# Kernel tuning notes

Measured on AMD Instinct MI355X. Metric: run time of the kernel, lower is better.

The kernel has to match this reference:

```python
import jax, jax.numpy as jnp
import numpy as np

N_NODES = 65536
N_EDGES = 1048576
HID = 128
NUM_FEAT = 128
NUM_LAYERS = 3
NUM_EXPERTS = 4
NUM_GRAPHS = 512
NUM_CLASSES = 10
TEMP = 0.1


def _hard_concrete(logits, key, temp=TEMP):
    u = jax.random.uniform(key, logits.shape, dtype=logits.dtype, minval=1e-6, maxval=1.0 - 1e-6)
    g = -jnp.log(-jnp.log(u + 1e-20) + 1e-20)
    y_soft = jax.nn.sigmoid((logits + g) / temp)
    y_hard = (y_soft > 0.5).astype(y_soft.dtype)
    # straight-through: forward hard, backward soft
    return y_hard + (y_soft - jax.lax.stop_gradient(y_soft))


def _gin_encoder(h, src, dst, w1, b1, w2, b2, eps, edge_weight=None):
    # GIN with optional scalar edge weights: agg = sum_{j->i} w_ij * h_j
    L = w1.shape[0]
    for l in range(L):
        msg = h[src]
        if edge_weight is not None:
            msg = msg * edge_weight[:, None]
        agg = jax.ops.segment_sum(msg, dst, num_segments=N_NODES)
        z = (1.0 + eps[l]) * h + agg
        z = jax.nn.relu(z @ w1[l] + b1[l]) @ w2[l] + b2[l]
        h = jax.nn.relu(z) if l < L - 1 else z
    return h


def _mean_pool(h, batch):
    s = jax.ops.segment_sum(h, batch, num_segments=NUM_GRAPHS)
    cnt = jax.ops.segment_sum(jnp.ones((h.shape[0], 1), h.dtype), batch, num_segments=NUM_GRAPHS)
    return s / jnp.maximum(cnt, 1.0)


def setup_inputs() -> dict:
    key = jax.random.key(0)
    ks = jax.random.split(key, 32)
    s = 0.05
    d = {}
    d['x'] = jax.random.normal(ks[0], (N_NODES, NUM_FEAT), dtype=jnp.float32)
    d['edge_index'] = jax.random.randint(ks[1], (2, N_EDGES), 0, N_NODES, dtype=jnp.int32)
    d['batch'] = jnp.sort(jax.random.randint(ks[2], (N_NODES,), 0, NUM_GRAPHS, dtype=jnp.int32))
    # causal encoder (layers stacked; F == HID so shapes are uniform)
    d['cw1'] = jax.random.normal(ks[3], (NUM_LAYERS, HID, HID), dtype=jnp.float32) * s
    d['cb1'] = jnp.zeros((NUM_LAYERS, HID), jnp.float32)
    d['cw2'] = jax.random.normal(ks[4], (NUM_LAYERS, HID, HID), dtype=jnp.float32) * s
    d['cb2'] = jnp.zeros((NUM_LAYERS, HID), jnp.float32)
    d['ceps'] = jnp.zeros((NUM_LAYERS,), jnp.float32)
    # classifier encoder
    d['kw1'] = jax.random.normal(ks[5], (NUM_LAYERS, HID, HID), dtype=jnp.float32) * s
    d['kb1'] = jnp.zeros((NUM_LAYERS, HID), jnp.float32)
    d['kw2'] = jax.random.normal(ks[6], (NUM_LAYERS, HID, HID), dtype=jnp.float32) * s
    d['kb2'] = jnp.zeros((NUM_LAYERS, HID), jnp.float32)
    d['keps'] = jnp.zeros((NUM_LAYERS,), jnp.float32)
    # per-expert node mask MLPs: HID -> HID -> 1
    d['nm_w1'] = jax.random.normal(ks[7], (NUM_EXPERTS, HID, HID), dtype=jnp.float32) * s
    d['nm_b1'] = jnp.zeros((NUM_EXPERTS, HID), jnp.float32)
    d['nm_w2'] = jax.random.normal(ks[8], (NUM_EXPERTS, HID, 1), dtype=jnp.float32) * s
    d['nm_b2'] = jnp.zeros((NUM_EXPERTS, 1), jnp.float32)
    # per-expert edge mask MLPs: 2*HID -> HID -> 1
    d['em_w1'] = jax.random.normal(ks[9], (NUM_EXPERTS, 2 * HID, HID), dtype=jnp.float32) * s
    d['em_b1'] = jnp.zeros((NUM_EXPERTS, HID), jnp.float32)
    d['em_w2'] = jax.random.normal(ks[10], (NUM_EXPERTS, HID, 1), dtype=jnp.float32) * s
    d['em_b2'] = jnp.zeros((NUM_EXPERTS, 1), jnp.float32)
    # per-expert feat mask MLPs: HID -> HID -> NUM_FEAT
    d['fm_w1'] = jax.random.normal(ks[11], (NUM_EXPERTS, HID, HID), dtype=jnp.float32) * s
    d['fm_b1'] = jnp.zeros((NUM_EXPERTS, HID), jnp.float32)
    d['fm_w2'] = jax.random.normal(ks[12], (NUM_EXPERTS, HID, NUM_FEAT), dtype=jnp.float32) * s
    d['fm_b2'] = jnp.zeros((NUM_EXPERTS, NUM_FEAT), jnp.float32)
    # per-expert classifiers
    d['cls_w'] = jax.random.normal(ks[13], (NUM_EXPERTS, HID, NUM_CLASSES), dtype=jnp.float32) * s
    d['cls_b'] = jnp.zeros((NUM_EXPERTS, NUM_CLASSES), jnp.float32)
    return d


def reference(x, edge_index, batch, cw1, cb1, cw2, cb2, ceps, kw1, kb1, kw2, kb2, keps,
              nm_w1, nm_b1, nm_w2, nm_b2, em_w1, em_b1, em_w2, em_b2,
              fm_w1, fm_b1, fm_w2, fm_b2, cls_w, cls_b):
    src, dst = edge_index[0], edge_index[1]
    Z = _gin_encoder(x, src, dst, cw1, cb1, cw2, cb2, ceps)  # [N, HID]
    edge_feat = jnp.concatenate([Z[src], Z[dst]], axis=1)     # [E, 2*HID]
    base_key = jax.random.key(42)
    node_masks, edge_masks, feat_masks = [], [], []
    h_stable_list, expert_logits = [], []
    for k in range(NUM_EXPERTS):
        kk = jax.random.split(jax.random.fold_in(base_key, k), 3)
        nl = jax.nn.relu(Z @ nm_w1[k] + nm_b1[k]) @ nm_w2[k] + nm_b2[k]          # [N,1]
        el = jax.nn.relu(edge_feat @ em_w1[k] + em_b1[k]) @ em_w2[k] + em_b2[k]  # [E,1]
        fl = jax.nn.relu(Z @ fm_w1[k] + fm_b1[k]) @ fm_w2[k] + fm_b2[k]          # [N,F]
        node_mask = _hard_concrete(nl, kk[0])
        edge_mask = _hard_concrete(el, kk[1])
        feat_mask = _hard_concrete(fl, kk[2])
        node_masks.append(node_mask)
        edge_masks.append(edge_mask)
        feat_masks.append(feat_mask)
        masked_x = x * node_mask * feat_mask
        ew = edge_mask[:, 0]
        masked_Z = _gin_encoder(masked_x, src, dst, kw1, kb1, kw2, kb2, keps, edge_weight=ew)
        h_st = _mean_pool(masked_Z, batch)                                        # [G, HID]
        h_stable_list.append(h_st)
        expert_logits.append(h_st @ cls_w[k] + cls_b[k])
    node_masks = jnp.stack(node_masks, axis=1)       # [N, K, 1]
    edge_masks = jnp.stack(edge_masks, axis=1)       # [E, K, 1]
    feat_masks = jnp.stack(feat_masks, axis=1)       # [N, K, F]
    h_stable = jnp.stack(h_stable_list, axis=1)      # [G, K, HID]
    expert_logits = jnp.stack(expert_logits, axis=1) # [G, K, C]
    h_orig = _mean_pool(Z, batch)                    # [G, HID]
    return expert_logits, h_stable, h_orig, node_masks, edge_masks, feat_masks
```

## Files before the change

kernel.cpp:

```cpp
#include <hip/hip_runtime.h>
#include <stdint.h>

#define N_NODESC 65536
#define N_EDGESC 1048576
#define HIDC 128
#define NUM_GRAPHSC 512
#define NUM_CLASSESC 10
#define NUM_EXPERTSC 4
#define NUM_LAYERSC 3

static const size_t NH = (size_t)N_NODESC * HIDC;

typedef __attribute__((ext_vector_type(8))) short short8v;
typedef __attribute__((ext_vector_type(4))) float float4v;

__host__ __device__ __forceinline__ uint32_t rotl32(uint32_t v, int r) {
  return (v << r) | (v >> (32 - r));
}
__host__ __device__ inline void threefry2x32(uint32_t k0, uint32_t k1,
                                             uint32_t x0, uint32_t x1,
                                             uint32_t* o0, uint32_t* o1) {
  uint32_t k2 = k0 ^ k1 ^ 0x1BD11BDAu;
  x0 += k0; x1 += k1;
#define TF_R(r) x0 += x1; x1 = rotl32(x1, r); x1 ^= x0;
  TF_R(13) TF_R(15) TF_R(26) TF_R(6)
  x0 += k1; x1 += k2 + 1u;
  TF_R(17) TF_R(29) TF_R(16) TF_R(24)
  x0 += k2; x1 += k0 + 2u;
  TF_R(13) TF_R(15) TF_R(26) TF_R(6)
  x0 += k0; x1 += k1 + 3u;
  TF_R(17) TF_R(29) TF_R(16) TF_R(24)
  x0 += k1; x1 += k2 + 4u;
  TF_R(13) TF_R(15) TF_R(26) TF_R(6)
  x0 += k2; x1 += k0 + 5u;
#undef TF_R
  *o0 = x0; *o1 = x1;
}

__device__ __forceinline__ float uniform_from_bits(uint32_t b) {
  float f = __uint_as_float((b >> 9) | 0x3f800000u) - 1.0f;
  const float mn = 1e-6f;
  const float mx = 1.0f - 1e-6f;
  return fmaxf(mn, __fadd_rn(__fmul_rn(f, __fsub_rn(mx, mn)), mn));
}

__device__ __forceinline__ float hc_decide(float l, uint32_t key0, uint32_t key1,
                                           uint32_t i) {
  uint32_t o0, o1;
  threefry2x32(key0, key1, 0u, i, &o0, &o1);
  float u = uniform_from_bits(o0 ^ o1);
  float tf = -__logf(u);
  float gf = -__logf(tf);
  float margf = l + gf;
  if (fabsf(margf) > 1e-4f) return (margf > 0.0f) ? 1.0f : 0.0f;
  float t32 = (float)(-log((double)u));
  float g32 = (float)(-log((double)t32));
  float m32 = __fadd_rn(l, g32);
  float q = m32 / 0.1f;
  float e32 = (float)exp(-(double)q);
  float den = __fadd_rn(1.0f, e32);
  float s = 1.0f / den;
  return (s > 0.5f) ? 1.0f : 0.0f;
}

__device__ __forceinline__ float bf2f(unsigned short u) {
  return __uint_as_float(((uint32_t)u) << 16);
}
__device__ __forceinline__ unsigned short f2bf(float v) {
  uint32_t u = __float_as_uint(v);
  return (unsigned short)((u + 0x7FFFu + ((u >> 16) & 1u)) >> 16);
}

__global__ void khist(const int* __restrict__ dst, int* __restrict__ deg) {
  int e = blockIdx.x * 256 + threadIdx.x;
  if (e < N_EDGESC) atomicAdd(&deg[dst[e]], 1);
}

__global__ void kscan(const int* __restrict__ deg, int* __restrict__ offs) {
  __shared__ int part[1024];
  int t = threadIdx.x;
  int base = t * 64;
  int s = 0;
  for (int i = 0; i < 64; ++i) s += deg[base + i];
  part[t] = s;
  __syncthreads();
  for (int off = 1; off < 1024; off <<= 1) {
    int v = 0;
    if (t >= off) v = part[t - off];
    __syncthreads();
    part[t] += v;
    __syncthreads();
  }
  int run = part[t] - s;
  for (int i = 0; i < 64; ++i) {
    int d = deg[base + i];
    offs[base + i] = run;
    run += d;
  }
  if (t == 1023) offs[N_NODESC] = run;
}

__global__ void kfill(const int* __restrict__ src, const int* __restrict__ dst,
                      int* __restrict__ curs, int* __restrict__ csr_src,
                      int* __restrict__ csr_eid) {
  int e = blockIdx.x * 256 + threadIdx.x;
  if (e >= N_EDGESC) return;
  int d = dst[e];
  int p = atomicAdd(&curs[d], 1);
  csr_src[p] = src[e];
  csr_eid[p] = e;
}

__global__ void ksort(const int* __restrict__ offs, int* __restrict__ csr_src,
                      int* __restrict__ csr_eid) {
  int n = blockIdx.x * 256 + threadIdx.x;
  if (n >= N_NODESC) return;
  int s = offs[n], e = offs[n + 1];
  for (int i = s + 1; i < e; ++i) {
    int ke = csr_eid[i], ks = csr_src[i];
    int j = i - 1;
    while (j >= s && csr_eid[j] > ke) {
      csr_eid[j + 1] = csr_eid[j];
      csr_src[j + 1] = csr_src[j];
      --j;
    }
    csr_eid[j + 1] = ke;
    csr_src[j + 1] = ks;
  }
}

__global__ void kbounds(const int* __restrict__ batch, int* __restrict__ bounds) {
  int g = threadIdx.x;
  int lo = 0, hi = N_NODESC;
  while (lo < hi) {
    int mid = (lo + hi) >> 1;
    if (batch[mid] < g) lo = mid + 1; else hi = mid;
  }
  bounds[g] = lo;
  if (g == 0) bounds[NUM_GRAPHSC] = N_NODESC;
}

__global__ void gather_z(const float* __restrict__ hin,
                         const int* __restrict__ offs,
                         const int* __restrict__ csr_src,
                         const float* __restrict__ epsArr, int l,
                         float* __restrict__ zout) {
  int gt = blockIdx.x * blockDim.x + threadIdx.x;
  int n = gt >> 6;
  int lane = gt & 63;
  if (n >= N_NODESC) return;
  int s = offs[n], e = offs[n + 1];
  float ax = 0.f, ay = 0.f;
  int i = s;
  for (; i + 4 <= e; i += 4) {
    int s0 = csr_src[i], s1 = csr_src[i + 1], s2 = csr_src[i + 2], s3 = csr_src[i + 3];
    const float2 v0 = *(const float2*)&hin[(size_t)s0 * HIDC + lane * 2];
    const float2 v1 = *(const float2*)&hin[(size_t)s1 * HIDC + lane * 2];
    const float2 v2 = *(const float2*)&hin[(size_t)s2 * HIDC + lane * 2];
    const float2 v3 = *(const float2*)&hin[(size_t)s3 * HIDC + lane * 2];
    ax = __fadd_rn(ax, v0.x); ay = __fadd_rn(ay, v0.y);
    ax = __fadd_rn(ax, v1.x); ay = __fadd_rn(ay, v1.y);
    ax = __fadd_rn(ax, v2.x); ay = __fadd_rn(ay, v2.y);
    ax = __fadd_rn(ax, v3.x); ay = __fadd_rn(ay, v3.y);
  }
  for (; i < e; ++i) {
    int sn = csr_src[i];
    const float2 v = *(const float2*)&hin[(size_t)sn * HIDC + lane * 2];
    ax = __fadd_rn(ax, v.x);
    ay = __fadd_rn(ay, v.y);
  }
  float ep = __fadd_rn(1.0f, epsArr[l]);
  const float2 hv = *(const float2*)&hin[(size_t)n * HIDC + lane * 2];
  ax = __fadd_rn(__fmul_rn(ep, hv.x), ax);
  ay = __fadd_rn(__fmul_rn(ep, hv.y), ay);
  float2 o; o.x = ax; o.y = ay;
  *(float2*)&zout[(size_t)n * HIDC + lane * 2] = o;
}

__device__ __forceinline__ int MXOR(int m) { return (m * 4) ^ ((m & 96) >> 1); }
__device__ __forceinline__ int KX(int k) { return ((k >> 2) & 7) << 4; }

template <typename EPI>
__device__ __forceinline__ void gemm_core(const float* __restrict__ Xf,
                                          const float* __restrict__ W,
                                          const float* __restrict__ bias,
                                          int doRelu, int tile, EPI epi) {
  __shared__ char sXb[64 * 512];
  __shared__ char sWb[64 * 512];
  const int tid = threadIdx.x;
  const size_t base = (size_t)tile * HIDC * HIDC;
  const int tm = (tid >> 4) << 3;
  const int tn = (tid & 15) << 3;
  const int xA = MXOR(tm), xA2 = MXOR(tm + 4);
  const int xB = MXOR(tn), xB2 = MXOR(tn + 4);

  float acc[8][8];
#pragma unroll
  for (int i = 0; i < 8; ++i)
#pragma unroll
    for (int j = 0; j < 8; ++j) acc[i][j] = 0.0f;

  for (int kh = 0; kh < 2; ++kh) {
    __syncthreads();
#pragma unroll
    for (int i = 0; i < 8; ++i) {
      int idx = tid + 256 * i;
      int m = idx >> 4;
      int kq = (idx & 15) * 4;
      float4 v = *(const float4*)(Xf + base + (size_t)m * HIDC + kh * 64 + kq);
      int mo = MXOR(m);
      *(float*)(sXb + (kq + 0) * 512 + (mo ^ KX(kq + 0))) = v.x;
      *(float*)(sXb + (kq + 1) * 512 + (mo ^ KX(kq + 1))) = v.y;
      *(float*)(sXb + (kq + 2) * 512 + (mo ^ KX(kq + 2))) = v.z;
      *(float*)(sXb + (kq + 3) * 512 + (mo ^ KX(kq + 3))) = v.w;
    }
#pragma unroll
    for (int i = 0; i < 8; ++i) {
      int idx = tid + 256 * i;
      int kk = idx >> 5;
      int n0 = (idx & 31) * 4;
      float4 v = *(const float4*)(W + (size_t)(kh * 64 + kk) * HIDC + n0);
      *(float4*)(sWb + kk * 512 + (MXOR(n0) ^ KX(kk))) = v;
    }
    __syncthreads();

#pragma unroll 4
    for (int kk = 0; kk < 64; ++kk) {
      int kx = KX(kk);
      float4 a0 = *(const float4*)(sXb + kk * 512 + (xA ^ kx));
      float4 a1 = *(const float4*)(sXb + kk * 512 + (xA2 ^ kx));
      float4 b0 = *(const float4*)(sWb + kk * 512 + (xB ^ kx));
      float4 b1 = *(const float4*)(sWb + kk * 512 + (xB2 ^ kx));
      float a[8] = {a0.x, a0.y, a0.z, a0.w, a1.x, a1.y, a1.z, a1.w};
      float b[8] = {b0.x, b0.y, b0.z, b0.w, b1.x, b1.y, b1.z, b1.w};
#pragma unroll
      for (int i = 0; i < 8; ++i)
#pragma unroll
        for (int j = 0; j < 8; ++j) acc[i][j] = fmaf(a[i], b[j], acc[i][j]);
    }
  }

  float bvals[8];
#pragma unroll
  for (int j = 0; j < 8; ++j) bvals[j] = bias ? bias[tn + j] : 0.0f;
#pragma unroll
  for (int i = 0; i < 8; ++i) {
    float r[8];
#pragma unroll
    for (int j = 0; j < 8; ++j) {
      float v = __fadd_rn(acc[i][j], bvals[j]);
      if (doRelu) v = fmaxf(v, 0.0f);
      r[j] = v;
    }
    epi(tile * HIDC + tm + i, tn, r);
  }
}

__global__ __launch_bounds__(256, 2)
void gemm_f32(const float* __restrict__ X, const float* __restrict__ W,
              const float* __restrict__ bias, float* __restrict__ O, int doRelu) {
  gemm_core(X, W, bias, doRelu, blockIdx.x,
            [&](int row, int tn, const float* r) {
              float* orow = O + (size_t)row * HIDC + tn;
              *(float4*)&orow[0] = *(const float4*)&r[0];
              *(float4*)&orow[4] = *(const float4*)&r[4];
            });
}

__global__ __launch_bounds__(256, 2)
void gemm_f32x4(const float* __restrict__ X,
                const float* W0, const float* W1, const float* W2, const float* W3,
                const float* b0, const float* b1,
                float* o0, float* o1, float* o2, float* o3) {
  int slice = blockIdx.x >> 9;
  int tile = blockIdx.x & 511;
  const float* W; const float* bias; float* O; int relu;
  if (slice == 0)      { W = W0; bias = b0; O = o0; relu = 1; }
  else if (slice == 1) { W = W1; bias = b1; O = o1; relu = 1; }
  else if (slice == 2) { W = W2; bias = nullptr; O = o2; relu = 0; }
  else                 { W = W3; bias = nullptr; O = o3; relu = 0; }
  gemm_core(X, W, bias, relu, tile,
            [&](int row, int tn, const float* r) {
              float* orow = O + (size_t)row * HIDC + tn;
              *(float4*)&orow[0] = *(const float4*)&r[0];
              *(float4*)&orow[4] = *(const float4*)&r[4];
            });
}

__global__ __launch_bounds__(256, 2)
void gemm_feat(const float* __restrict__ X, const float* __restrict__ W,
               const float* __restrict__ bias, uint32_t key0, uint32_t key1,
               float* __restrict__ outFeat ) {
  gemm_core(X, W, bias, 0, blockIdx.x,
            [&](int row, int tn, const float* r) {
              float d[8];
#pragma unroll
              for (int j = 0; j < 8; ++j)
                d[j] = hc_decide(r[j], key0, key1,
                                 (uint32_t)(row * HIDC + tn + j));
              float* orow = outFeat + (size_t)row * (NUM_EXPERTSC * HIDC) + tn;
              *(float4*)&orow[0] = *(const float4*)&d[0];
              *(float4*)&orow[4] = *(const float4*)&d[4];
            });
}

__global__ void kprepW(const float* __restrict__ kw1, const float* __restrict__ kw2,
                       unsigned short* __restrict__ Wt) {
  int t = blockIdx.x * 256 + threadIdx.x;
  int mat = t >> 11;
  int r = t & 2047;
  int n = r >> 4;
  int kkc = r & 15;
  const float* W = (mat < 3) ? (kw1 + (size_t)mat * HIDC * HIDC)
                             : (kw2 + (size_t)(mat - 3) * HIDC * HIDC);
  unsigned short pk[8];
#pragma unroll
  for (int j = 0; j < 8; ++j)
    pk[j] = f2bf(W[(size_t)(kkc * 8 + j) * HIDC + n]);
  *(uint4*)(Wt + (size_t)mat * HIDC * HIDC + (size_t)n * HIDC + kkc * 8) =
      *(uint4*)pk;
}

__global__ __launch_bounds__(256, 2)
void gemm_mfma2(const unsigned short* __restrict__ Xpool,
                const unsigned short* __restrict__ Wt1,
                const unsigned short* __restrict__ Wt2,
                const float* __restrict__ bias1, const float* __restrict__ bias2,
                unsigned short* __restrict__ Opool, int doRelu2) {
  __shared__ unsigned short sX[128 * 128];
  __shared__ unsigned short sW[128 * 128];
  const int tid = threadIdx.x;
  const int kex = blockIdx.x >> 9;
  const int tile = blockIdx.x & 511;
  const unsigned short* X = Xpool + (size_t)kex * NH + (size_t)tile * HIDC * HIDC;
  unsigned short* O = Opool + (size_t)kex * NH + (size_t)tile * HIDC * HIDC;

  const int lane = tid & 63;
  const int wid = tid >> 6;
  const int wm = wid * 32;
  const int lrow = lane & 15;
  const int lk = (lane >> 4) * 4;
  union FU { uint2 u2[2]; short8v s8; };

#pragma unroll
  for (int i = 0; i < 8; ++i) {
    int idx = tid + 256 * i;
    int r = idx >> 4;
    int cc = idx & 15;
    uint4 vx = *(const uint4*)(X + (size_t)r * HIDC + cc * 8);
    uint4 vw = *(const uint4*)(Wt1 + (size_t)r * HIDC + cc * 8);
    int sc = (cc ^ (r & 7)) * 8;
    *(uint4*)(sX + r * HIDC + sc) = vx;
    *(uint4*)(sW + r * HIDC + sc) = vw;
  }
  __syncthreads();

  float4v acc[2][8];
#pragma unroll
  for (int rt = 0; rt < 2; ++rt)
#pragma unroll
    for (int nt = 0; nt < 8; ++nt) acc[rt][nt] = (float4v)0.0f;

  for (int kc = 0; kc < 128; kc += 32) {
    int kb = kc + lk;
    short8v afr[2], bfr[8];
#pragma unroll
    for (int rt = 0; rt < 2; ++rt) {
      int row = wm + rt * 16 + lrow;
      const unsigned short* basep = sX + row * HIDC;
      int s0 = (((kb) >> 3) ^ (row & 7)) * 8 + (kb & 7);
      int s1 = (((kb + 16) >> 3) ^ (row & 7)) * 8 + (kb & 7);
      FU u;
      u.u2[0] = *(const uint2*)(basep + s0);
      u.u2[1] = *(const uint2*)(basep + s1);
      afr[rt] = u.s8;
    }
#pragma unroll
    for (int nt = 0; nt < 8; ++nt) {
      int row = nt * 16 + lrow;
      const unsigned short* basep = sW + row * HIDC;
      int s0 = (((kb) >> 3) ^ (row & 7)) * 8 + (kb & 7);
      int s1 = (((kb + 16) >> 3) ^ (row & 7)) * 8 + (kb & 7);
      FU u;
      u.u2[0] = *(const uint2*)(basep + s0);
      u.u2[1] = *(const uint2*)(basep + s1);
      bfr[nt] = u.s8;
    }
#pragma unroll
    for (int rt = 0; rt < 2; ++rt)
#pragma unroll
      for (int nt = 0; nt < 8; ++nt)
        acc[rt][nt] = __builtin_amdgcn_mfma_f32_16x16x32_bf16(
            afr[rt], bfr[nt], acc[rt][nt], 0, 0, 0);
  }
  __syncthreads();

#pragma unroll
  for (int nt = 0; nt < 8; ++nt) {
    float bv = bias1[nt * 16 + lrow];
#pragma unroll
    for (int rt = 0; rt < 2; ++rt) {
#pragma unroll
      for (int j = 0; j < 4; ++j) {
        float v = fmaxf(acc[rt][nt][j] + bv, 0.0f);
        int row = wm + rt * 16 + (lane >> 4) * 4 + j;
        int col = nt * 16 + lrow;
        int sc = (((col >> 3) ^ (row & 7)) * 8) + (col & 7);
        sX[row * HIDC + sc] = f2bf(v);
      }
    }
  }
#pragma unroll
  for (int i = 0; i < 8; ++i) {
    int idx = tid + 256 * i;
    int r = idx >> 4;
    int cc = idx & 15;
    uint4 vw = *(const uint4*)(Wt2 + (size_t)r * HIDC + cc * 8);
    *(uint4*)(sW + r * HIDC + ((cc ^ (r & 7)) * 8)) = vw;
  }
  __syncthreads();

#pragma unroll
  for (int rt = 0; rt < 2; ++rt)
#pragma unroll
    for (int nt = 0; nt < 8; ++nt) acc[rt][nt] = (float4v)0.0f;

  for (int kc = 0; kc < 128; kc += 32) {
    int kb = kc + lk;
    short8v afr[2], bfr[8];
#pragma unroll
    for (int rt = 0; rt < 2; ++rt) {
      int row = wm + rt * 16 + lrow;
      const unsigned short* basep = sX + row * HIDC;
      int s0 = (((kb) >> 3) ^ (row & 7)) * 8 + (kb & 7);
      int s1 = (((kb + 16) >> 3) ^ (row & 7)) * 8 + (kb & 7);
      FU u;
      u.u2[0] = *(const uint2*)(basep + s0);
      u.u2[1] = *(const uint2*)(basep + s1);
      afr[rt] = u.s8;
    }
#pragma unroll
    for (int nt = 0; nt < 8; ++nt) {
      int row = nt * 16 + lrow;
      const unsigned short* basep = sW + row * HIDC;
      int s0 = (((kb) >> 3) ^ (row & 7)) * 8 + (kb & 7);
      int s1 = (((kb + 16) >> 3) ^ (row & 7)) * 8 + (kb & 7);
      FU u;
      u.u2[0] = *(const uint2*)(basep + s0);
      u.u2[1] = *(const uint2*)(basep + s1);
      bfr[nt] = u.s8;
    }
#pragma unroll
    for (int rt = 0; rt < 2; ++rt)
#pragma unroll
      for (int nt = 0; nt < 8; ++nt)
        acc[rt][nt] = __builtin_amdgcn_mfma_f32_16x16x32_bf16(
            afr[rt], bfr[nt], acc[rt][nt], 0, 0, 0);
  }

#pragma unroll
  for (int nt = 0; nt < 8; ++nt) {
    float bv = bias2[nt * 16 + lrow];
#pragma unroll
    for (int rt = 0; rt < 2; ++rt) {
#pragma unroll
      for (int j = 0; j < 4; ++j) {
        float v = acc[rt][nt][j] + bv;
        if (doRelu2) v = fmaxf(v, 0.0f);
        int row = wm + rt * 16 + (lane >> 4) * 4 + j;
        O[(size_t)row * HIDC + nt * 16 + lrow] = f2bf(v);
      }
    }
  }
}

__global__ void rowdot(const float* __restrict__ X, const float* __restrict__ w,
                       const float* __restrict__ bptr, uint32_t key0, uint32_t key1,
                       float* __restrict__ outp) {
  int gt = blockIdx.x * blockDim.x + threadIdx.x;
  int row = gt >> 6, lane = gt & 63;
  if (row >= N_NODESC) return;
  const float2 x = *(const float2*)&X[(size_t)row * HIDC + lane * 2];
  const float2 ww = *(const float2*)&w[lane * 2];
  float p = x.x * ww.x + x.y * ww.y;
#pragma unroll
  for (int m = 32; m; m >>= 1) p += __shfl_xor(p, m, 64);
  if (lane == 0) {
    float l = p + bptr[0];
    outp[(size_t)row * NUM_EXPERTSC] = hc_decide(l, key0, key1, (uint32_t)row);
  }
}

__global__ void edge_csrK(const float* __restrict__ A, const float* __restrict__ Bm,
                          const float* __restrict__ b1, const float* __restrict__ w2,
                          const float* __restrict__ b2,
                          const int* __restrict__ offs, const int* __restrict__ csr_src,
                          const int* __restrict__ csr_eid,
                          uint32_t key0, uint32_t key1,
                          float* __restrict__ outp, unsigned char* __restrict__ mcsr) {
  int n = blockIdx.x * 4 + (threadIdx.x >> 6);
  int lane = threadIdx.x & 63;
  int g = lane >> 4;
  int gl = lane & 15;
  const float4* Bv = (const float4*)&Bm[(size_t)n * HIDC + gl * 8];
  float4 b_lo = Bv[0], b_hi = Bv[1];
  float4 bb_lo = *(const float4*)&b1[gl * 8];
  float4 bb_hi = *(const float4*)&b1[gl * 8 + 4];
  float4 w_lo = *(const float4*)&w2[gl * 8];
  float4 w_hi = *(const float4*)&w2[gl * 8 + 4];
  float bscalar = b2[0];
  int s = offs[n], e = offs[n + 1];
  for (int i = s; i < e; i += 4) {
    int cnt = e - i; if (cnt > 4) cnt = 4;
    float p = 0.0f;
    if (g < cnt) {
      int sg = csr_src[i + g];
      const float4* Av = (const float4*)&A[(size_t)sg * HIDC + gl * 8];
      float4 a_lo = Av[0], a_hi = Av[1];
      float h;
      h = fmaxf(__fadd_rn(__fadd_rn(a_lo.x, b_lo.x), bb_lo.x), 0.0f); p = fmaf(h, w_lo.x, p);
      h = fmaxf(__fadd_rn(__fadd_rn(a_lo.y, b_lo.y), bb_lo.y), 0.0f); p = fmaf(h, w_lo.y, p);
      h = fmaxf(__fadd_rn(__fadd_rn(a_lo.z, b_lo.z), bb_lo.z), 0.0f); p = fmaf(h, w_lo.z, p);
      h = fmaxf(__fadd_rn(__fadd_rn(a_lo.w, b_lo.w), bb_lo.w), 0.0f); p = fmaf(h, w_lo.w, p);
      h = fmaxf(__fadd_rn(__fadd_rn(a_hi.x, b_hi.x), bb_hi.x), 0.0f); p = fmaf(h, w_hi.x, p);
      h = fmaxf(__fadd_rn(__fadd_rn(a_hi.y, b_hi.y), bb_hi.y), 0.0f); p = fmaf(h, w_hi.y, p);
      h = fmaxf(__fadd_rn(__fadd_rn(a_hi.z, b_hi.z), bb_hi.z), 0.0f); p = fmaf(h, w_hi.z, p);
      h = fmaxf(__fadd_rn(__fadd_rn(a_hi.w, b_hi.w), bb_hi.w), 0.0f); p = fmaf(h, w_hi.w, p);
    }
    p += __shfl_xor(p, 1, 16);
    p += __shfl_xor(p, 2, 16);
    p += __shfl_xor(p, 4, 16);
    p += __shfl_xor(p, 8, 16);
    if (g < cnt && gl == 0) {
      int eid = csr_eid[i + g];
      float l = p + bscalar;
      float mval = hc_decide(l, key0, key1, (uint32_t)eid);
      outp[(size_t)eid * NUM_EXPERTSC] = mval;
      mcsr[i + g] = (unsigned char)mval;
    }
  }
}

__global__ void kmaskxB(const float* __restrict__ x, const float* __restrict__ nmaskb,
                        const float* __restrict__ fmaskb,
                        unsigned short* __restrict__ hbpool) {
  int k = blockIdx.x >> 13;
  int t = (blockIdx.x & 8191) * 256 + threadIdx.x;
  int n = t >> 5;
  int q = (t & 31) << 2;
  float nm = nmaskb[(size_t)n * NUM_EXPERTSC + k];
  float4 xv = *(const float4*)&x[(size_t)n * HIDC + q];
  float4 fv = *(const float4*)&fmaskb[(size_t)n * (NUM_EXPERTSC * HIDC) + k * HIDC + q];
  ushort2 p0, p1;
  p0.x = f2bf(xv.x * nm * fv.x); p0.y = f2bf(xv.y * nm * fv.y);
  p1.x = f2bf(xv.z * nm * fv.z); p1.y = f2bf(xv.w * nm * fv.w);
  uint2 pk; pk.x = (uint32_t)p0.x | ((uint32_t)p0.y << 16);
  pk.y = (uint32_t)p1.x | ((uint32_t)p1.y << 16);
  *(uint2*)(hbpool + (size_t)k * NH + (size_t)n * HIDC + q) = pk;
}

__global__ void gatherC(const unsigned short* __restrict__ hpool,
                        const int* __restrict__ offs,
                        const int* __restrict__ csr_src,
                        const unsigned char* __restrict__ mcsr,
                        const float* __restrict__ epsArr, int l,
                        unsigned short* __restrict__ aggpool) {
  int gid = blockIdx.x * 4 + (threadIdx.x >> 6);
  int lane = threadIdx.x & 63;
  int k = gid >> 16;
  int n = gid & 65535;
  const unsigned short* h = hpool + (size_t)k * NH;
  const unsigned char* mc = mcsr + (size_t)k * N_EDGESC;
  int s = offs[n], e = offs[n + 1];
  float ax = 0.f, ay = 0.f;
  for (int base = s; base < e; base += 64) {
    int j = base + lane;
    int valid = (j < e);
    int keep = valid ? (mc[j] != 0) : 0;
    int srcj = valid ? csr_src[j] : 0;
    unsigned long long ball = __ballot(keep);
    while (ball) {
      int l0 = -1, l1 = -1, l2 = -1, l3 = -1;
      l0 = __ffsll((unsigned long long)ball) - 1; ball &= ball - 1;
      if (ball) { l1 = __ffsll((unsigned long long)ball) - 1; ball &= ball - 1; }
      if (ball) { l2 = __ffsll((unsigned long long)ball) - 1; ball &= ball - 1; }
      if (ball) { l3 = __ffsll((unsigned long long)ball) - 1; ball &= ball - 1; }
      int s0 = __shfl(srcj, l0, 64);
      int s1 = (l1 >= 0) ? __shfl(srcj, l1, 64) : 0;
      int s2 = (l2 >= 0) ? __shfl(srcj, l2, 64) : 0;
      int s3 = (l3 >= 0) ? __shfl(srcj, l3, 64) : 0;
      uint32_t v0 = *(const uint32_t*)(h + (size_t)s0 * HIDC + lane * 2);
      uint32_t v1 = (l1 >= 0) ? *(const uint32_t*)(h + (size_t)s1 * HIDC + lane * 2) : 0;
      uint32_t v2 = (l2 >= 0) ? *(const uint32_t*)(h + (size_t)s2 * HIDC + lane * 2) : 0;
      uint32_t v3 = (l3 >= 0) ? *(const uint32_t*)(h + (size_t)s3 * HIDC + lane * 2) : 0;
      ax += __uint_as_float(v0 << 16); ay += __uint_as_float(v0 & 0xFFFF0000u);
      if (l1 >= 0) { ax += __uint_as_float(v1 << 16); ay += __uint_as_float(v1 & 0xFFFF0000u); }
      if (l2 >= 0) { ax += __uint_as_float(v2 << 16); ay += __uint_as_float(v2 & 0xFFFF0000u); }
      if (l3 >= 0) { ax += __uint_as_float(v3 << 16); ay += __uint_as_float(v3 & 0xFFFF0000u); }
    }
  }
  float ep = 1.0f + epsArr[l];
  uint32_t hv = *(const uint32_t*)(h + (size_t)n * HIDC + lane * 2);
  ax = fmaf(ep, __uint_as_float(hv << 16), ax);
  ay = fmaf(ep, __uint_as_float(hv & 0xFFFF0000u), ay);
  uint32_t pk = (uint32_t)f2bf(ax) | ((uint32_t)f2bf(ay) << 16);
  *(uint32_t*)(aggpool + (size_t)k * NH + (size_t)n * HIDC + lane * 2) = pk;
}

__global__ void pool(const float* __restrict__ h, const int* __restrict__ bounds,
                     float* __restrict__ outp, int rowStride) {
  int g = blockIdx.x, j = threadIdx.x;
  int s = bounds[g], e = bounds[g + 1];
  float acc = 0.0f;
  for (int i = s; i < e; ++i) acc = __fadd_rn(acc, h[(size_t)i * HIDC + j]);
  int cnt = e - s; if (cnt < 1) cnt = 1;
  outp[(size_t)g * rowStride + j] = acc / (float)cnt;
}

__global__ void poolB(const unsigned short* __restrict__ hbpool,
                      const int* __restrict__ bounds, float* __restrict__ outp) {
  int k = blockIdx.x >> 9;
  int g = blockIdx.x & 511;
  int j = threadIdx.x;
  const unsigned short* h = hbpool + (size_t)k * NH;
  int s = bounds[g], e = bounds[g + 1];
  float acc = 0.0f;
  for (int i = s; i < e; ++i) acc += bf2f(h[(size_t)i * HIDC + j]);
  int cnt = e - s; if (cnt < 1) cnt = 1;
  outp[(size_t)g * (NUM_EXPERTSC * HIDC) + k * HIDC + j] = acc / (float)cnt;
}

__global__ void kclsB(const float* __restrict__ hst, const float* __restrict__ w,
                      const float* __restrict__ b, float* __restrict__ outp) {
  int k = blockIdx.x >> 9;
  int g = blockIdx.x & 511;
  int c = threadIdx.x;
  if (c >= NUM_CLASSESC) return;
  float acc = 0.0f;
  for (int j = 0; j < HIDC; ++j)
    acc = __fadd_rn(acc, __fmul_rn(hst[(size_t)g * (NUM_EXPERTSC * HIDC) + k * HIDC + j],
                                   w[(size_t)k * HIDC * NUM_CLASSESC + j * NUM_CLASSESC + c]));
  outp[(size_t)g * (NUM_EXPERTSC * NUM_CLASSESC) + k * NUM_CLASSESC + c] =
      acc + b[k * NUM_CLASSESC + c];
}

extern "C" void kernel_launch(void* const* d_in, const int* in_sizes, int n_in,
                              void* d_out, int out_size, void* d_ws, size_t ws_size,
                              hipStream_t stream) {
  const float* x    = (const float*)d_in[0];
  const int* eidx   = (const int*)d_in[1];
  const int* batch  = (const int*)d_in[2];
  const float* cw1  = (const float*)d_in[3];
  const float* cb1  = (const float*)d_in[4];
  const float* cw2  = (const float*)d_in[5];
  const float* cb2  = (const float*)d_in[6];
  const float* ceps = (const float*)d_in[7];
  const float* kw1  = (const float*)d_in[8];
  const float* kb1  = (const float*)d_in[9];
  const float* kw2  = (const float*)d_in[10];
  const float* kb2  = (const float*)d_in[11];
  const float* keps = (const float*)d_in[12];
  const float* nm_w1 = (const float*)d_in[13];
  const float* nm_b1 = (const float*)d_in[14];
  const float* nm_w2 = (const float*)d_in[15];
  const float* nm_b2 = (const float*)d_in[16];
  const float* em_w1 = (const float*)d_in[17];
  const float* em_b1 = (const float*)d_in[18];
  const float* em_w2 = (const float*)d_in[19];
  const float* em_b2 = (const float*)d_in[20];
  const float* fm_w1 = (const float*)d_in[21];
  const float* fm_b1 = (const float*)d_in[22];
  const float* fm_w2 = (const float*)d_in[23];
  const float* fm_b2 = (const float*)d_in[24];
  const float* cls_w = (const float*)d_in[25];
  const float* cls_b = (const float*)d_in[26];

  const int* src = eidx;
  const int* dstp = eidx + N_EDGESC;
  float* out = (float*)d_out;

  const size_t OFF_HST    = 20480;
  const size_t OFF_HORIG  = 282624;
  const size_t OFF_NODE   = 348160;
  const size_t OFF_EDGE   = 610304;
  const size_t OFF_FEAT   = 4804608;

  float* P  = (float*)d_ws;
  float* Zf = P;
  float* t1 = P + NH;
  float* t2 = P + 2 * NH;
  float* t3 = P + 3 * NH;
  float* t4 = P + 4 * NH;
  unsigned short* hbB  = (unsigned short*)P;
  unsigned short* aggB = (unsigned short*)(P + 2 * NH);
  float* nl = P + 6 * NH;
  int* deg    = (int*)(nl + N_NODESC);
  int* offs   = deg + N_NODESC;
  int* curs   = offs + N_NODESC + 1;
  int* csr_s  = curs + N_NODESC;
  int* csr_e  = csr_s + N_EDGESC;
  int* bounds = csr_e + N_EDGESC;
  unsigned char* mcsr = (unsigned char*)(bounds + NUM_GRAPHSC + 3);
  unsigned short* Wt = (unsigned short*)(mcsr + 4 * (size_t)N_EDGESC + 64);

  uint32_t kk[NUM_EXPERTSC][3][2];
  for (int k = 0; k < NUM_EXPERTSC; ++k) {
    uint32_t f0, f1;
    threefry2x32(0u, 42u, 0u, (uint32_t)k, &f0, &f1);
    threefry2x32(f0, f1, 0u, 0u, &kk[k][0][0], &kk[k][0][1]);
    threefry2x32(f0, f1, 0u, 1u, &kk[k][1][0], &kk[k][1][1]);
    threefry2x32(f0, f1, 0u, 2u, &kk[k][2][0], &kk[k][2][1]);
  }

  hipMemsetAsync(deg, 0, N_NODESC * sizeof(int), stream);
  khist<<<N_EDGESC / 256, 256, 0, stream>>>(dstp, deg);
  kscan<<<1, 1024, 0, stream>>>(deg, offs);
  hipMemcpyAsync(curs, offs, N_NODESC * sizeof(int), hipMemcpyDeviceToDevice, stream);
  kfill<<<N_EDGESC / 256, 256, 0, stream>>>(src, dstp, curs, csr_s, csr_e);
  ksort<<<N_NODESC / 256, 256, 0, stream>>>(offs, csr_s, csr_e);
  kbounds<<<1, NUM_GRAPHSC, 0, stream>>>(batch, bounds);
  kprepW<<<48, 256, 0, stream>>>(kw1, kw2, Wt);

  const int GZ_GRID = N_NODESC * 64 / 256;
  const int GEMM_GRID = N_NODESC / HIDC;

  for (int l = 0; l < NUM_LAYERSC; ++l) {
    const float* hin = (l == 0) ? x : t1;
    gather_z<<<GZ_GRID, 256, 0, stream>>>(hin, offs, csr_s, ceps, l, t3);
    gemm_f32<<<GEMM_GRID, 256, 0, stream>>>(t3, cw1 + (size_t)l * HIDC * HIDC,
                                            cb1 + l * HIDC, t2, 1);
    gemm_f32<<<GEMM_GRID, 256, 0, stream>>>(t2, cw2 + (size_t)l * HIDC * HIDC,
                                            cb2 + l * HIDC,
                                            (l == NUM_LAYERSC - 1) ? Zf : t1,
                                            (l < NUM_LAYERSC - 1) ? 1 : 0);
  }
  pool<<<NUM_GRAPHSC, HIDC, 0, stream>>>(Zf, bounds, out + OFF_HORIG, HIDC);

  for (int k = 0; k < NUM_EXPERTSC; ++k) {
    gemm_f32x4<<<4 * GEMM_GRID, 256, 0, stream>>>(
        Zf,
        nm_w1 + (size_t)k * HIDC * HIDC, fm_w1 + (size_t)k * HIDC * HIDC,
        em_w1 + (size_t)k * 2 * HIDC * HIDC,
        em_w1 + (size_t)k * 2 * HIDC * HIDC + HIDC * HIDC,
        nm_b1 + k * HIDC, fm_b1 + k * HIDC,
        t1, t2, t3, t4);
    rowdot<<<GZ_GRID, 256, 0, stream>>>(t1, nm_w2 + (size_t)k * HIDC, nm_b2 + k,
                                        kk[k][0][0], kk[k][0][1], out + OFF_NODE + k);
    gemm_feat<<<GEMM_GRID, 256, 0, stream>>>(t2, fm_w2 + (size_t)k * HIDC * HIDC,
                                             fm_b2 + (size_t)k * HIDC,
                                             kk[k][2][0], kk[k][2][1],
                                             out + OFF_FEAT + (size_t)k * HIDC);
    edge_csrK<<<N_NODESC / 4, 256, 0, stream>>>(t3, t4, em_b1 + k * HIDC,
                                                em_w2 + (size_t)k * HIDC, em_b2 + k,
                                                offs, csr_s, csr_e,
                                                kk[k][1][0], kk[k][1][1],
                                                out + OFF_EDGE + k,
                                                mcsr + (size_t)k * N_EDGESC);
  }

  kmaskxB<<<4 * 8192, 256, 0, stream>>>(x, out + OFF_NODE, out + OFF_FEAT, hbB);
  for (int l = 0; l < NUM_LAYERSC; ++l) {
    gatherC<<<4 * GZ_GRID, 256, 0, stream>>>(hbB, offs, csr_s, mcsr, keps, l, aggB);
    gemm_mfma2<<<4 * GEMM_GRID, 256, 0, stream>>>(aggB,
                                                  Wt + (size_t)l * HIDC * HIDC,
                                                  Wt + (size_t)(3 + l) * HIDC * HIDC,
                                                  kb1 + l * HIDC, kb2 + l * HIDC,
                                                  hbB, (l < NUM_LAYERSC - 1) ? 1 : 0);
  }
  poolB<<<4 * NUM_GRAPHSC, HIDC, 0, stream>>>(hbB, bounds, out + OFF_HST);
  kclsB<<<4 * NUM_GRAPHSC, 64, 0, stream>>>(out + OFF_HST, cls_w, cls_b, out);
}
```

Before: 2.555 ms.

## Fuse node-mask rowdot into expert GEMM epilogue and halve GEMM smem tiles

The node-mask second layer (a 128-wide dot product plus hard-concrete decision) now runs inside the epilogue of the first-layer GEMM slice, using 16-lane shuffles. This removes the rowdot kernel and the write and re-read of its intermediate activation buffer. Separately, the fp32 GEMM core now stages K in 32-wide chunks instead of 64, halving shared memory, and launch bounds go to 4 blocks per CU for higher occupancy. The cost is twice as many barriers per tile and register pressure under the tighter launch bound.

```diff
diff --git a/kernel.cpp b/kernel.cpp
--- a/kernel.cpp
+++ b/kernel.cpp
@@ -185,8 +185,8 @@
                                           const float* __restrict__ W,
                                           const float* __restrict__ bias,
                                           int doRelu, int tile, EPI epi) {
-  __shared__ char sXb[64 * 512];
-  __shared__ char sWb[64 * 512];
+  __shared__ char sXb[32 * 512];
+  __shared__ char sWb[32 * 512];
   const int tid = threadIdx.x;
   const size_t base = (size_t)tile * HIDC * HIDC;
   const int tm = (tid >> 4) << 3;
@@ -200,14 +200,14 @@
 #pragma unroll
     for (int j = 0; j < 8; ++j) acc[i][j] = 0.0f;
 
-  for (int kh = 0; kh < 2; ++kh) {
+  for (int kh = 0; kh < 4; ++kh) {
     __syncthreads();
 #pragma unroll
-    for (int i = 0; i < 8; ++i) {
+    for (int i = 0; i < 4; ++i) {
       int idx = tid + 256 * i;
-      int m = idx >> 4;
-      int kq = (idx & 15) * 4;
-      float4 v = *(const float4*)(Xf + base + (size_t)m * HIDC + kh * 64 + kq);
+      int m = idx >> 3;
+      int kq = (idx & 7) * 4;
+      float4 v = *(const float4*)(Xf + base + (size_t)m * HIDC + kh * 32 + kq);
       int mo = MXOR(m);
       *(float*)(sXb + (kq + 0) * 512 + (mo ^ KX(kq + 0))) = v.x;
       *(float*)(sXb + (kq + 1) * 512 + (mo ^ KX(kq + 1))) = v.y;
@@ -215,17 +215,17 @@
       *(float*)(sXb + (kq + 3) * 512 + (mo ^ KX(kq + 3))) = v.w;
     }
 #pragma unroll
-    for (int i = 0; i < 8; ++i) {
+    for (int i = 0; i < 4; ++i) {
       int idx = tid + 256 * i;
       int kk = idx >> 5;
       int n0 = (idx & 31) * 4;
-      float4 v = *(const float4*)(W + (size_t)(kh * 64 + kk) * HIDC + n0);
+      float4 v = *(const float4*)(W + (size_t)(kh * 32 + kk) * HIDC + n0);
       *(float4*)(sWb + kk * 512 + (MXOR(n0) ^ KX(kk))) = v;
     }
     __syncthreads();
 
 #pragma unroll 4
-    for (int kk = 0; kk < 64; ++kk) {
+    for (int kk = 0; kk < 32; ++kk) {
       int kx = KX(kk);
       float4 a0 = *(const float4*)(sXb + kk * 512 + (xA ^ kx));
       float4 a1 = *(const float4*)(sXb + kk * 512 + (xA2 ^ kx));
@@ -256,7 +256,7 @@
   }
 }
 
-__global__ __launch_bounds__(256, 2)
+__global__ __launch_bounds__(256, 4)
 void gemm_f32(const float* __restrict__ X, const float* __restrict__ W,
               const float* __restrict__ bias, float* __restrict__ O, int doRelu) {
   gemm_core(X, W, bias, doRelu, blockIdx.x,
@@ -267,27 +267,51 @@
             });
 }
 
-__global__ __launch_bounds__(256, 2)
+__global__ __launch_bounds__(256, 4)
 void gemm_f32x4(const float* __restrict__ X,
                 const float* W0, const float* W1, const float* W2, const float* W3,
                 const float* b0, const float* b1,
-                float* o0, float* o1, float* o2, float* o3) {
+                const float* __restrict__ nw2, const float* __restrict__ nb2,
+                uint32_t key0, uint32_t key1, float* __restrict__ outNode,
+                float* o1, float* o2, float* o3) {
   int slice = blockIdx.x >> 9;
   int tile = blockIdx.x & 511;
-  const float* W; const float* bias; float* O; int relu;
-  if (slice == 0)      { W = W0; bias = b0; O = o0; relu = 1; }
-  else if (slice == 1) { W = W1; bias = b1; O = o1; relu = 1; }
-  else if (slice == 2) { W = W2; bias = nullptr; O = o2; relu = 0; }
-  else                 { W = W3; bias = nullptr; O = o3; relu = 0; }
-  gemm_core(X, W, bias, relu, tile,
-            [&](int row, int tn, const float* r) {
-              float* orow = O + (size_t)row * HIDC + tn;
-              *(float4*)&orow[0] = *(const float4*)&r[0];
-              *(float4*)&orow[4] = *(const float4*)&r[4];
-            });
-}
-
-__global__ __launch_bounds__(256, 2)
+  if (slice == 0) {
+    const int tn0 = (threadIdx.x & 15) << 3;
+    float w2v[8];
+#pragma unroll
+    for (int j = 0; j < 8; ++j) w2v[j] = nw2[tn0 + j];
+    float b2s = nb2[0];
+    gemm_core(X, W0, b0, 1, tile,
+              [&](int row, int tn, const float* r) {
+                float pd = 0.0f;
+#pragma unroll
+                for (int j = 0; j < 8; ++j) pd = fmaf(r[j], w2v[j], pd);
+                pd += __shfl_xor(pd, 1, 16);
+                pd += __shfl_xor(pd, 2, 16);
+                pd += __shfl_xor(pd, 4, 16);
+                pd += __shfl_xor(pd, 8, 16);
+                if ((threadIdx.x & 15) == (row & 7)) {
+                  float l = pd + b2s;
+                  outNode[(size_t)row * NUM_EXPERTSC] =
+                      hc_decide(l, key0, key1, (uint32_t)row);
+                }
+              });
+  } else {
+    const float* W; const float* bias; float* O; int relu;
+    if (slice == 1)      { W = W1; bias = b1; O = o1; relu = 1; }
+    else if (slice == 2) { W = W2; bias = nullptr; O = o2; relu = 0; }
+    else                 { W = W3; bias = nullptr; O = o3; relu = 0; }
+    gemm_core(X, W, bias, relu, tile,
+              [&](int row, int tn, const float* r) {
+                float* orow = O + (size_t)row * HIDC + tn;
+                *(float4*)&orow[0] = *(const float4*)&r[0];
+                *(float4*)&orow[4] = *(const float4*)&r[4];
+              });
+  }
+}
+
+__global__ __launch_bounds__(256, 4)
 void gemm_feat(const float* __restrict__ X, const float* __restrict__ W,
                const float* __restrict__ bias, uint32_t key0, uint32_t key1,
                float* __restrict__ outFeat ) {
@@ -471,23 +495,6 @@
         O[(size_t)row * HIDC + nt * 16 + lrow] = f2bf(v);
       }
     }
-  }
-}
-
-__global__ void rowdot(const float* __restrict__ X, const float* __restrict__ w,
-                       const float* __restrict__ bptr, uint32_t key0, uint32_t key1,
-                       float* __restrict__ outp) {
-  int gt = blockIdx.x * blockDim.x + threadIdx.x;
-  int row = gt >> 6, lane = gt & 63;
-  if (row >= N_NODESC) return;
-  const float2 x = *(const float2*)&X[(size_t)row * HIDC + lane * 2];
-  const float2 ww = *(const float2*)&w[lane * 2];
-  float p = x.x * ww.x + x.y * ww.y;
-#pragma unroll
-  for (int m = 32; m; m >>= 1) p += __shfl_xor(p, m, 64);
-  if (lane == 0) {
-    float l = p + bptr[0];
-    outp[(size_t)row * NUM_EXPERTSC] = hc_decide(l, key0, key1, (uint32_t)row);
   }
 }
 
@@ -702,6 +709,7 @@
   int* bounds = csr_e + N_EDGESC;
   unsigned char* mcsr = (unsigned char*)(bounds + NUM_GRAPHSC + 3);
   unsigned short* Wt = (unsigned short*)(mcsr + 4 * (size_t)N_EDGESC + 64);
+  (void)t1;
 
   uint32_t kk[NUM_EXPERTSC][3][2];
   for (int k = 0; k < NUM_EXPERTSC; ++k) {
@@ -725,13 +733,13 @@
   const int GEMM_GRID = N_NODESC / HIDC;
 
   for (int l = 0; l < NUM_LAYERSC; ++l) {
-    const float* hin = (l == 0) ? x : t1;
+    const float* hin = (l == 0) ? x : t2;
     gather_z<<<GZ_GRID, 256, 0, stream>>>(hin, offs, csr_s, ceps, l, t3);
     gemm_f32<<<GEMM_GRID, 256, 0, stream>>>(t3, cw1 + (size_t)l * HIDC * HIDC,
-                                            cb1 + l * HIDC, t2, 1);
-    gemm_f32<<<GEMM_GRID, 256, 0, stream>>>(t2, cw2 + (size_t)l * HIDC * HIDC,
+                                            cb1 + l * HIDC, t4, 1);
+    gemm_f32<<<GEMM_GRID, 256, 0, stream>>>(t4, cw2 + (size_t)l * HIDC * HIDC,
                                             cb2 + l * HIDC,
-                                            (l == NUM_LAYERSC - 1) ? Zf : t1,
+                                            (l == NUM_LAYERSC - 1) ? Zf : t2,
                                             (l < NUM_LAYERSC - 1) ? 1 : 0);
   }
   pool<<<NUM_GRAPHSC, HIDC, 0, stream>>>(Zf, bounds, out + OFF_HORIG, HIDC);
@@ -743,9 +751,9 @@
         em_w1 + (size_t)k * 2 * HIDC * HIDC,
         em_w1 + (size_t)k * 2 * HIDC * HIDC + HIDC * HIDC,
         nm_b1 + k * HIDC, fm_b1 + k * HIDC,
-        t1, t2, t3, t4);
-    rowdot<<<GZ_GRID, 256, 0, stream>>>(t1, nm_w2 + (size_t)k * HIDC, nm_b2 + k,
-                                        kk[k][0][0], kk[k][0][1], out + OFF_NODE + k);
+        nm_w2 + (size_t)k * HIDC, nm_b2 + k,
+        kk[k][0][0], kk[k][0][1], out + OFF_NODE + k,
+        t2, t3, t4);
     gemm_feat<<<GEMM_GRID, 256, 0, stream>>>(t2, fm_w2 + (size_t)k * HIDC * HIDC,
                                              fm_b2 + (size_t)k * HIDC,
                                              kk[k][2][0], kk[k][2][1],
```

New measurement: 2.593 ms. Within noise of the previous version (+1.5%).
